# Kernel tuning notes

Measured on AMD Instinct MI355X. Metric: run time of the kernel, lower is better.

## Reference

```python
import jax, jax.numpy as jnp
import numpy as np

N = 10000      # num nodes
E = 320000     # num edges
IN = 256       # in_dim
MP = 256       # mp_width
FL = 512       # fl_width
OUT = 64       # out_dim


def setup_inputs() -> dict:
    key = jax.random.key(0)
    ks = jax.random.split(key, 20)
    inp = {}
    inp["x"] = jax.random.normal(ks[0], (N, IN), dtype=jnp.float32)
    inp["edge_index"] = jax.random.randint(ks[1], (2, E), 0, N, dtype=jnp.int64)
    # iMP (frozen) linear layers: weight ~ N(0, 1) per nn.init.normal_(std=1.0)
    inp["mp_w0"] = jax.random.normal(ks[2], (IN, MP), dtype=jnp.float32)
    inp["mp_b0"] = jax.random.uniform(ks[3], (MP,), minval=-1.0, maxval=1.0) / np.sqrt(IN)
    inp["mp_w1"] = jax.random.normal(ks[4], (MP, MP), dtype=jnp.float32)
    inp["mp_b1"] = jax.random.uniform(ks[5], (MP,), minval=-1.0, maxval=1.0) / np.sqrt(MP)
    inp["mp_w2"] = jax.random.normal(ks[6], (MP, MP), dtype=jnp.float32)
    inp["mp_b2"] = jax.random.uniform(ks[7], (MP,), minval=-1.0, maxval=1.0) / np.sqrt(MP)
    # FC layers (torch default Linear init scale ~ 1/sqrt(fan_in))
    inp["fc_w0"] = jax.random.normal(ks[8], (MP, FL), dtype=jnp.float32) / np.sqrt(MP)
    inp["fc_b0"] = jnp.zeros((FL,), dtype=jnp.float32)
    inp["fc_w1"] = jax.random.normal(ks[9], (FL, FL), dtype=jnp.float32) / np.sqrt(FL)
    inp["fc_b1"] = jnp.zeros((FL,), dtype=jnp.float32)
    # injection projections
    inp["inj_w0"] = jax.random.normal(ks[10], (MP, FL), dtype=jnp.float32) / np.sqrt(MP)
    inp["inj_b0"] = jnp.zeros((FL,), dtype=jnp.float32)
    inp["inj_w1"] = jax.random.normal(ks[11], (MP, FL), dtype=jnp.float32) / np.sqrt(MP)
    inp["inj_b1"] = jnp.zeros((FL,), dtype=jnp.float32)
    inp["alpha"] = jnp.array(1.0, dtype=jnp.float32)
    inp["out_w"] = jax.random.normal(ks[12], (FL, OUT), dtype=jnp.float32) / np.sqrt(FL)
    inp["out_b"] = jnp.zeros((OUT,), dtype=jnp.float32)
    return inp


def _imp(x, w, b, row, col, deg_inv):
    # h = relu(W x); h /= deg; Ah = scatter_add over row of h[col]
    h = jax.nn.relu(x @ w + b) * deg_inv[:, None]      # [N, out]
    return jnp.zeros_like(h).at[row].add(h[col])       # gather + scatter-add


def reference(x, edge_index, mp_w0, mp_b0, mp_w1, mp_b1, mp_w2, mp_b2,
              fc_w0, fc_b0, fc_w1, fc_b1, inj_w0, inj_b0, inj_w1, inj_b1,
              alpha, out_w, out_b):
    row, col = edge_index[0], edge_index[1]
    deg = jax.ops.segment_sum(jnp.ones((E,), x.dtype), col, num_segments=N)
    # nodes with deg==0 never appear in col so clamping does not change output
    deg_inv = 1.0 / jnp.maximum(deg, 1.0)

    h = _imp(x, mp_w0, mp_b0, row, col, deg_inv)
    h = _imp(h, mp_w1, mp_b1, row, col, deg_inv)
    h = _imp(h, mp_w2, mp_b2, row, col, deg_inv)

    x_inject = h
    h = alpha * (jax.nn.relu(h) @ fc_w0 + fc_b0) + (x_inject @ inj_w0 + inj_b0)
    h = alpha * (jax.nn.relu(h) @ fc_w1 + fc_b1) + (x_inject @ inj_w1 + inj_b1)
    return h @ out_w + out_b
```

## Files before the change

kernel.cpp:

```cpp
#include <hip/hip_runtime.h>

#define N_NODES 10000
#define N_EDGES 320000
#define MPAD 10112
#define NBIN 10048
#define CHUNK 2048
#define NCH 157
#define CAP 128
#define PREP_BLOCKS 512
#define PREP_TOT 1148480L

typedef unsigned short u16;
typedef short bf16x8 __attribute__((ext_vector_type(8)));
typedef float f32x4 __attribute__((ext_vector_type(4)));

__device__ __forceinline__ u16 f2b(float f) {
  unsigned u = __builtin_bit_cast(unsigned, f);
  unsigned r = u + 0x7fffu + ((u >> 16) & 1u);
  return (u16)(r >> 16);
}
__device__ __forceinline__ unsigned pack2(float a, float b) {
  return (unsigned)f2b(a) | ((unsigned)f2b(b) << 16);
}
__device__ __forceinline__ float blo(unsigned u) { return __builtin_bit_cast(float, u << 16); }
__device__ __forceinline__ float bhi(unsigned u) { return __builtin_bit_cast(float, u & 0xffff0000u); }

struct PP {
  const float *x; const int *ei;
  const float *w0, *w1, *w2, *fcw0, *injw0, *fcw1, *injw1, *outw;
  const float *fcb0, *injb0, *fcb1, *injb1, *alpha, *outb;
  u16 *xb, *w0t, *w1t, *w2t, *wc1t, *wft;
  float *bias1, *bf;
  unsigned *histRC;
};

__global__ __launch_bounds__(256) void prep_hist(PP P) {
  __shared__ unsigned sh[NBIN];
  const int tid = threadIdx.x, bid = blockIdx.x;
  const float alpha = P.alpha[0];

  if (bid < NCH) {
    for (int i = tid; i < NBIN; i += 256) sh[i] = 0;
    __syncthreads();
    const int e0 = bid * CHUNK;
    for (int j = tid; j < CHUNK; j += 256) {
      int e = e0 + j;
      if (e < N_EDGES) {
        atomicAdd(&sh[P.ei[e]], 1u);
        atomicAdd(&sh[P.ei[N_EDGES + e]], 65536u);
      }
    }
    __syncthreads();
    for (int i = tid; i < NBIN; i += 256)
      P.histRC[(size_t)bid * NBIN + i] = sh[i];
    return;
  }

  const long stride = (long)PREP_BLOCKS * 256;
  for (long ii = (long)(bid - NCH) * 256 + tid; ii < PREP_TOT; ii += stride) {
    long i = ii;
    if (i < 640000L) {
      float4 v = ((const float4*)P.x)[i];
      uint2 o;
      o.x = pack2(v.x, v.y);
      o.y = pack2(v.z, v.w);
      *(uint2*)(P.xb + 4 * i) = o;
      continue;
    }
    i -= 640000L;
    if (i < 65536) { P.w0t[i] = f2b(P.w0[(i & 255) * 256 + (i >> 8)]); continue; }
    i -= 65536;
    if (i < 65536) { P.w1t[i] = f2b(P.w1[(i & 255) * 256 + (i >> 8)]); continue; }
    i -= 65536;
    if (i < 65536) { P.w2t[i] = f2b(P.w2[(i & 255) * 256 + (i >> 8)]); continue; }
    i -= 65536;
    if (i < 262144) {
      int n = (int)(i >> 9), k = (int)(i & 511);
      float v = (k < 256) ? alpha * P.fcw0[k * 512 + n] : P.injw0[(k - 256) * 512 + n];
      P.wc1t[i] = f2b(v); continue;
    }
    i -= 262144;
    if (i < 49152) {
      int n = (int)(i & 63), k = (int)(i >> 6);
      float acc = 0.f;
      if (k < 512) {
        const float* fr = P.fcw1 + (size_t)k * 512;
#pragma unroll 8
        for (int j = 0; j < 512; ++j) acc += fr[j] * P.outw[j * 64 + n];
        acc *= alpha;
      } else {
        const float* ir = P.injw1 + (size_t)(k - 512) * 512;
#pragma unroll 8
        for (int j = 0; j < 512; ++j) acc += ir[j] * P.outw[j * 64 + n];
      }
      P.wft[n * 768 + k] = f2b(acc);
      continue;
    }
    i -= 49152;
    if (i < 64) {
      float acc = P.outb[i];
#pragma unroll 8
      for (int j = 0; j < 512; ++j)
        acc += (alpha * P.fcb1[j] + P.injb1[j]) * P.outw[j * 64 + i];
      P.bf[i] = acc;
      continue;
    }
    i -= 64;
    if (i < 512) { P.bias1[i] = alpha * P.fcb0[i] + P.injb0[i]; continue; }
  }
}

__global__ __launch_bounds__(64) void col_scan(const unsigned* __restrict__ histRC,
                                               u16* __restrict__ chunkoff,
                                               int* __restrict__ cnt,
                                               float* __restrict__ deg_inv) {
  int r = blockIdx.x * 64 + threadIdx.x;
  if (r >= MPAD) return;
  if (r >= NBIN) { deg_inv[r] = 1.0f; return; }
  unsigned run = 0;
#pragma unroll 8
  for (int ch = 0; ch < NCH; ++ch) {
    chunkoff[(size_t)ch * NBIN + r] = (u16)(run & 0xffffu);
    run += histRC[(size_t)ch * NBIN + r];
  }
  int cr = (int)(run & 0xffffu);
  int dg = (int)(run >> 16);
  cnt[r] = cr;
  deg_inv[r] = 1.0f / (float)(dg > 1 ? dg : 1);
}

__global__ __launch_bounds__(256) void place_edges(const int* __restrict__ ei,
                                                   const u16* __restrict__ chunkoff,
                                                   int* __restrict__ csr) {
  __shared__ int cur[NBIN];
  const int ch = blockIdx.x, t = threadIdx.x;
  const u16* co = chunkoff + (size_t)ch * NBIN;
  for (int i = t; i < NBIN; i += 256) cur[i] = co[i];
  __syncthreads();
  const int e0 = ch * CHUNK;
#pragma unroll
  for (int j = 0; j < CHUNK; j += 256) {
    int e = e0 + j + t;
    if (e < N_EDGES) {
      int r = ei[e];
      int c = ei[N_EDGES + e];
      int rank = atomicAdd(&cur[r], 1);
      if (rank < CAP) csr[r * CAP + rank] = c;
    }
  }
}

template<int K, bool RELU, bool SCALE, bool F32OUT>
__global__ __launch_bounds__(128) void gemm64(
    const u16* __restrict__ A, int lda,
    const u16* __restrict__ Bt,
    const float* __restrict__ bias,
    const float* __restrict__ scale,
    u16* __restrict__ Cb, float* __restrict__ Cf, int ldc)
{
  __shared__ u16 As[64 * 72];
  __shared__ u16 Bs[64 * 72];
  const int tid = threadIdx.x;
  const int m0 = blockIdx.x * 64;
  const int n0 = blockIdx.y * 64;
  const int wave = tid >> 6;
  const int lane = tid & 63;
  const int wr = wave * 32;
  const int lm = lane & 15;
  const int koff = (lane >> 4) * 8;

  const int srow = tid >> 2;
  const int scol = (tid & 3) * 16;
  const u16* Ag0 = A + (size_t)(m0 + srow) * lda + scol;
  const u16* Ag1 = A + (size_t)(m0 + srow + 32) * lda + scol;
  const u16* Bg0 = Bt + (size_t)(n0 + srow) * K + scol;
  const u16* Bg1 = Bt + (size_t)(n0 + srow + 32) * K + scol;
  u16* Asw0 = &As[srow * 72 + scol];
  u16* Asw1 = &As[(srow + 32) * 72 + scol];
  u16* Bsw0 = &Bs[srow * 72 + scol];
  u16* Bsw1 = &Bs[(srow + 32) * 72 + scol];

  f32x4 acc[2][4] = {};

  int4 pa0 = *(const int4*)(Ag0),     pa1 = *(const int4*)(Ag0 + 8);
  int4 pa2 = *(const int4*)(Ag1),     pa3 = *(const int4*)(Ag1 + 8);
  int4 pb0 = *(const int4*)(Bg0),     pb1 = *(const int4*)(Bg0 + 8);
  int4 pb2 = *(const int4*)(Bg1),     pb3 = *(const int4*)(Bg1 + 8);

#pragma unroll
  for (int kb = 0; kb < K; kb += 64) {
    __syncthreads();
    *(int4*)Asw0 = pa0; *(int4*)(Asw0 + 8) = pa1;
    *(int4*)Asw1 = pa2; *(int4*)(Asw1 + 8) = pa3;
    *(int4*)Bsw0 = pb0; *(int4*)(Bsw0 + 8) = pb1;
    *(int4*)Bsw1 = pb2; *(int4*)(Bsw1 + 8) = pb3;
    __syncthreads();
    if (kb + 64 < K) {
      pa0 = *(const int4*)(Ag0 + kb + 64); pa1 = *(const int4*)(Ag0 + kb + 72);
      pa2 = *(const int4*)(Ag1 + kb + 64); pa3 = *(const int4*)(Ag1 + kb + 72);
      pb0 = *(const int4*)(Bg0 + kb + 64); pb1 = *(const int4*)(Bg0 + kb + 72);
      pb2 = *(const int4*)(Bg1 + kb + 64); pb3 = *(const int4*)(Bg1 + kb + 72);
    }
#pragma unroll
    for (int ks = 0; ks < 2; ++ks) {
      bf16x8 af[2], bf[4];
#pragma unroll
      for (int mi = 0; mi < 2; ++mi)
        af[mi] = *(const bf16x8*)&As[(wr + mi * 16 + lm) * 72 + ks * 32 + koff];
#pragma unroll
      for (int ni = 0; ni < 4; ++ni)
        bf[ni] = *(const bf16x8*)&Bs[(ni * 16 + lm) * 72 + ks * 32 + koff];
#pragma unroll
      for (int mi = 0; mi < 2; ++mi)
#pragma unroll
        for (int ni = 0; ni < 4; ++ni)
          acc[mi][ni] = __builtin_amdgcn_mfma_f32_16x16x32_bf16(af[mi], bf[ni], acc[mi][ni], 0, 0, 0);
    }
  }

  const int q4 = (lane >> 4) * 4;
#pragma unroll
  for (int mi = 0; mi < 2; ++mi) {
#pragma unroll
    for (int ni = 0; ni < 4; ++ni) {
      const int gc = n0 + ni * 16 + lm;
      const float bv = bias[gc];
#pragma unroll
      for (int r = 0; r < 4; ++r) {
        const int gr = m0 + wr + mi * 16 + q4 + r;
        float v = acc[mi][ni][r] + bv;
        if (RELU) v = fmaxf(v, 0.f);
        if (SCALE) v *= scale[gr];
        if (F32OUT) {
          if (gr < N_NODES) Cf[(size_t)gr * ldc + gc] = v;
        } else {
          Cb[(size_t)gr * ldc + gc] = f2b(v);
        }
      }
    }
  }
}

__global__ __launch_bounds__(256) void aggregate(
    const u16* __restrict__ tmp, const int* __restrict__ cnt,
    const int* __restrict__ csr, u16* __restrict__ out0,
    u16* __restrict__ A1, u16* __restrict__ A2, int mode)
{
  const int wv = threadIdx.x >> 6;
  const int lane = threadIdx.x & 63;
  const int r = blockIdx.x * 4 + wv;
  const int half = lane >> 5;
  const int q = lane & 31;
  const int beg = r * CAP, end = beg + cnt[r];
  const size_t feat = (size_t)q * 16;
  const char* tb = (const char*)tmp;

  float s0 = 0.f, s1 = 0.f, s2 = 0.f, s3 = 0.f, s4 = 0.f, s5 = 0.f, s6 = 0.f, s7 = 0.f;
  int i = beg;
  for (; i + 8 <= end; i += 8) {
    uint4 v[4];
#pragma unroll
    for (int j = 0; j < 4; ++j)
      v[j] = *(const uint4*)(tb + (size_t)csr[i + 2 * j + half] * 512 + feat);
#pragma unroll
    for (int j = 0; j < 4; ++j) {
      s0 += blo(v[j].x); s1 += bhi(v[j].x); s2 += blo(v[j].y); s3 += bhi(v[j].y);
      s4 += blo(v[j].z); s5 += bhi(v[j].z); s6 += blo(v[j].w); s7 += bhi(v[j].w);
    }
  }
  for (; i < end; i += 2) {
    int id = i + half;
    if (id < end) {
      uint4 v = *(const uint4*)(tb + (size_t)csr[id] * 512 + feat);
      s0 += blo(v.x); s1 += bhi(v.x); s2 += blo(v.y); s3 += bhi(v.y);
      s4 += blo(v.z); s5 += bhi(v.z); s6 += blo(v.w); s7 += bhi(v.w);
    }
  }
  const int src = lane ^ 32;
  s0 += __shfl(s0, src, 64); s1 += __shfl(s1, src, 64);
  s2 += __shfl(s2, src, 64); s3 += __shfl(s3, src, 64);
  s4 += __shfl(s4, src, 64); s5 += __shfl(s5, src, 64);
  s6 += __shfl(s6, src, 64); s7 += __shfl(s7, src, 64);

  if (half == 0) {
    uint4 pv;
    pv.x = pack2(s0, s1); pv.y = pack2(s2, s3);
    pv.z = pack2(s4, s5); pv.w = pack2(s6, s7);
    if (mode == 0) {
      *(uint4*)((char*)out0 + (size_t)r * 512 + feat) = pv;
    } else {
      uint4 pr;
      pr.x = pack2(fmaxf(s0, 0.f), fmaxf(s1, 0.f));
      pr.y = pack2(fmaxf(s2, 0.f), fmaxf(s3, 0.f));
      pr.z = pack2(fmaxf(s4, 0.f), fmaxf(s5, 0.f));
      pr.w = pack2(fmaxf(s6, 0.f), fmaxf(s7, 0.f));
      *(uint4*)((char*)A1 + (size_t)r * 1024 + feat) = pr;
      *(uint4*)((char*)A1 + (size_t)r * 1024 + 512 + feat) = pv;
      *(uint4*)((char*)A2 + (size_t)r * 1536 + 1024 + feat) = pv;
    }
  }
}

extern "C" void kernel_launch(void* const* d_in, const int* in_sizes, int n_in,
                              void* d_out, int out_size, void* d_ws, size_t ws_size,
                              hipStream_t stream) {
  const int* ei = (const int*)d_in[1];

  char* p = (char*)d_ws;
  auto carve = [&](size_t bytes) -> void* {
    void* r = (void*)p;
    p += (bytes + 255) & ~(size_t)255;
    return r;
  };
  unsigned* histRC  = (unsigned*)carve((size_t)NCH * NBIN * 4);
  u16*    chunkoff  = (u16*)carve((size_t)NCH * NBIN * 2);
  int*    cnt       = (int*)carve(NBIN * 4);
  int*    csr       = (int*)carve((size_t)NBIN * CAP * 4);
  float*  deg_inv   = (float*)carve(MPAD * 4);
  float*  bias1     = (float*)carve(512 * 4);
  float*  bf        = (float*)carve(64 * 4);
  u16* xb   = (u16*)carve((size_t)MPAD * 256 * 2);
  u16* w0t  = (u16*)carve(65536 * 2);
  u16* w1t  = (u16*)carve(65536 * 2);
  u16* w2t  = (u16*)carve(65536 * 2);
  u16* wc1t = (u16*)carve(262144 * 2);
  u16* wft  = (u16*)carve(49152 * 2);
  u16* tmp  = (u16*)carve((size_t)MPAD * 256 * 2);
  u16* h    = (u16*)carve((size_t)MPAD * 256 * 2);
  u16* cat1 = (u16*)carve((size_t)MPAD * 512 * 2);
  u16* cat2 = (u16*)carve((size_t)MPAD * 768 * 2);

  PP pp;
  pp.x = (const float*)d_in[0];
  pp.ei = ei;
  pp.w0 = (const float*)d_in[2];
  pp.w1 = (const float*)d_in[4];
  pp.w2 = (const float*)d_in[6];
  pp.fcw0 = (const float*)d_in[8];
  pp.fcw1 = (const float*)d_in[10];
  pp.injw0 = (const float*)d_in[12];
  pp.injw1 = (const float*)d_in[14];
  pp.outw = (const float*)d_in[17];
  pp.fcb0 = (const float*)d_in[9];
  pp.injb0 = (const float*)d_in[13];
  pp.fcb1 = (const float*)d_in[11];
  pp.injb1 = (const float*)d_in[15];
  pp.alpha = (const float*)d_in[16];
  pp.outb = (const float*)d_in[18];
  pp.xb = xb; pp.w0t = w0t; pp.w1t = w1t; pp.w2t = w2t;
  pp.wc1t = wc1t; pp.wft = wft;
  pp.bias1 = bias1; pp.bf = bf;
  pp.histRC = histRC;

  const float* mp_b0 = (const float*)d_in[3];
  const float* mp_b1 = (const float*)d_in[5];
  const float* mp_b2 = (const float*)d_in[7];
  float* out = (float*)d_out;

  prep_hist<<<NCH + PREP_BLOCKS, 256, 0, stream>>>(pp);
  col_scan<<<MPAD / 64, 64, 0, stream>>>(histRC, chunkoff, cnt, deg_inv);
  place_edges<<<NCH, 256, 0, stream>>>(ei, chunkoff, csr);

  dim3 gmp(MPAD / 64, 4), gfc(MPAD / 64, 8), go(MPAD / 64, 1);
  gemm64<256, true, true, false><<<gmp, 128, 0, stream>>>(xb, 256, w0t, mp_b0, deg_inv, tmp, nullptr, 256);
  aggregate<<<2500, 256, 0, stream>>>(tmp, cnt, csr, h, nullptr, nullptr, 0);
  gemm64<256, true, true, false><<<gmp, 128, 0, stream>>>(h, 256, w1t, mp_b1, deg_inv, tmp, nullptr, 256);
  aggregate<<<2500, 256, 0, stream>>>(tmp, cnt, csr, h, nullptr, nullptr, 0);
  gemm64<256, true, true, false><<<gmp, 128, 0, stream>>>(h, 256, w2t, mp_b2, deg_inv, tmp, nullptr, 256);
  aggregate<<<2500, 256, 0, stream>>>(tmp, cnt, csr, nullptr, cat1, cat2, 1);
  gemm64<512, true, false, false><<<gfc, 128, 0, stream>>>(cat1, 512, wc1t, bias1, nullptr, cat2, nullptr, 768);
  gemm64<768, false, false, true><<<go, 128, 0, stream>>>(cat2, 768, wft, bf, nullptr, nullptr, out, 64);
}
```

Measured before the change: 245.1 us.

## Fuse edge placement with first MP GEMM into one launch; vectorize weight folding

Merges the place_edges kernel and the first message-passing GEMM into a single heterogeneous launch, with block IDs below NCH doing CSR placement and the rest computing GEMM tiles. Both parts share one dynamic-union shared buffer. This removes a launch and lets the two independent jobs overlap. Separately, the folded output-weight precompute now uses float4 loads and four partial accumulators to shorten the dependency chain. The cost is a large 40KB shared allocation for all blocks, which lowers GEMM-block occupancy, and 128-thread placement blocks.

```diff
diff --git a/kernel.cpp b/kernel.cpp
--- a/kernel.cpp
+++ b/kernel.cpp
@@ -82,17 +82,19 @@
     i -= 262144;
     if (i < 49152) {
       int n = (int)(i & 63), k = (int)(i >> 6);
-      float acc = 0.f;
-      if (k < 512) {
-        const float* fr = P.fcw1 + (size_t)k * 512;
-#pragma unroll 8
-        for (int j = 0; j < 512; ++j) acc += fr[j] * P.outw[j * 64 + n];
-        acc *= alpha;
-      } else {
-        const float* ir = P.injw1 + (size_t)(k - 512) * 512;
-#pragma unroll 8
-        for (int j = 0; j < 512; ++j) acc += ir[j] * P.outw[j * 64 + n];
+      const float* fr = (k < 512) ? P.fcw1 + (size_t)k * 512
+                                  : P.injw1 + (size_t)(k - 512) * 512;
+      float a0 = 0.f, a1 = 0.f, a2 = 0.f, a3 = 0.f;
+#pragma unroll 4
+      for (int j = 0; j < 512; j += 4) {
+        float4 f = *(const float4*)(fr + j);
+        a0 += f.x * P.outw[(j + 0) * 64 + n];
+        a1 += f.y * P.outw[(j + 1) * 64 + n];
+        a2 += f.z * P.outw[(j + 2) * 64 + n];
+        a3 += f.w * P.outw[(j + 3) * 64 + n];
       }
+      float acc = (a0 + a1) + (a2 + a3);
+      if (k < 512) acc *= alpha;
       P.wft[n * 768 + k] = f2b(acc);
       continue;
     }
@@ -129,40 +131,16 @@
   deg_inv[r] = 1.0f / (float)(dg > 1 ? dg : 1);
 }
 
-__global__ __launch_bounds__(256) void place_edges(const int* __restrict__ ei,
-                                                   const u16* __restrict__ chunkoff,
-                                                   int* __restrict__ csr) {
-  __shared__ int cur[NBIN];
-  const int ch = blockIdx.x, t = threadIdx.x;
-  const u16* co = chunkoff + (size_t)ch * NBIN;
-  for (int i = t; i < NBIN; i += 256) cur[i] = co[i];
-  __syncthreads();
-  const int e0 = ch * CHUNK;
-#pragma unroll
-  for (int j = 0; j < CHUNK; j += 256) {
-    int e = e0 + j + t;
-    if (e < N_EDGES) {
-      int r = ei[e];
-      int c = ei[N_EDGES + e];
-      int rank = atomicAdd(&cur[r], 1);
-      if (rank < CAP) csr[r * CAP + rank] = c;
-    }
-  }
-}
-
 template<int K, bool RELU, bool SCALE, bool F32OUT>
-__global__ __launch_bounds__(128) void gemm64(
+__device__ __forceinline__ void gemm_tile(
+    int m0, int n0,
     const u16* __restrict__ A, int lda,
     const u16* __restrict__ Bt,
     const float* __restrict__ bias,
     const float* __restrict__ scale,
-    u16* __restrict__ Cb, float* __restrict__ Cf, int ldc)
+    u16* __restrict__ Cb, float* __restrict__ Cf, int ldc,
+    u16* As, u16* Bs, int tid)
 {
-  __shared__ u16 As[64 * 72];
-  __shared__ u16 Bs[64 * 72];
-  const int tid = threadIdx.x;
-  const int m0 = blockIdx.x * 64;
-  const int n0 = blockIdx.y * 64;
   const int wave = tid >> 6;
   const int lane = tid & 63;
   const int wr = wave * 32;
@@ -239,6 +217,57 @@
       }
     }
   }
+}
+
+template<int K, bool RELU, bool SCALE, bool F32OUT>
+__global__ __launch_bounds__(128) void gemm64(
+    const u16* __restrict__ A, int lda,
+    const u16* __restrict__ Bt,
+    const float* __restrict__ bias,
+    const float* __restrict__ scale,
+    u16* __restrict__ Cb, float* __restrict__ Cf, int ldc)
+{
+  __shared__ u16 As[64 * 72];
+  __shared__ u16 Bs[64 * 72];
+  gemm_tile<K, RELU, SCALE, F32OUT>(blockIdx.x * 64, blockIdx.y * 64,
+                                    A, lda, Bt, bias, scale, Cb, Cf, ldc,
+                                    As, Bs, threadIdx.x);
+}
+
+__global__ __launch_bounds__(128) void place_gemm(
+    const int* __restrict__ ei, const u16* __restrict__ chunkoff,
+    int* __restrict__ csr,
+    const u16* __restrict__ xb, const u16* __restrict__ w0t,
+    const float* __restrict__ mp_b0, const float* __restrict__ deg_inv,
+    u16* __restrict__ tmp)
+{
+  __shared__ __align__(16) char smem[NBIN * 4];
+  const int bid = blockIdx.x, tid = threadIdx.x;
+
+  if (bid < NCH) {
+    int* cur = (int*)smem;
+    const u16* co = chunkoff + (size_t)bid * NBIN;
+    for (int i = tid; i < NBIN; i += 128) cur[i] = co[i];
+    __syncthreads();
+    const int e0 = bid * CHUNK;
+    for (int j = 0; j < CHUNK; j += 128) {
+      int e = e0 + j + tid;
+      if (e < N_EDGES) {
+        int r = ei[e];
+        int c = ei[N_EDGES + e];
+        int rank = atomicAdd(&cur[r], 1);
+        if (rank < CAP) csr[r * CAP + rank] = c;
+      }
+    }
+    return;
+  }
+
+  const int t = bid - NCH;
+  u16* As = (u16*)smem;
+  u16* Bs = (u16*)(smem + 9216);
+  gemm_tile<256, true, true, false>((t % 158) * 64, (t / 158) * 64,
+                                    xb, 256, w0t, mp_b0, deg_inv,
+                                    tmp, nullptr, 256, As, Bs, tid);
 }
 
 __global__ __launch_bounds__(256) void aggregate(
@@ -359,10 +388,10 @@
 
   prep_hist<<<NCH + PREP_BLOCKS, 256, 0, stream>>>(pp);
   col_scan<<<MPAD / 64, 64, 0, stream>>>(histRC, chunkoff, cnt, deg_inv);
-  place_edges<<<NCH, 256, 0, stream>>>(ei, chunkoff, csr);
+  place_gemm<<<NCH + 632, 128, 0, stream>>>(ei, chunkoff, csr,
+                                            xb, w0t, mp_b0, deg_inv, tmp);
 
   dim3 gmp(MPAD / 64, 4), gfc(MPAD / 64, 8), go(MPAD / 64, 1);
-  gemm64<256, true, true, false><<<gmp, 128, 0, stream>>>(xb, 256, w0t, mp_b0, deg_inv, tmp, nullptr, 256);
   aggregate<<<2500, 256, 0, stream>>>(tmp, cnt, csr, h, nullptr, nullptr, 0);
   gemm64<256, true, true, false><<<gmp, 128, 0, stream>>>(h, 256, w1t, mp_b1, deg_inv, tmp, nullptr, 256);
   aggregate<<<2500, 256, 0, stream>>>(tmp, cnt, csr, h, nullptr, nullptr, 0);
```

New measurement: 240.1 us. 1.02x faster.
